# Kernel optimization log

Measured on AMD Instinct MI355X. Metric: run time of the kernel, lower is better.

## Reference

```python
import jax, jax.numpy as jnp
import numpy as np

B, C, H, W = 8, 256, 64, 64
EPS = 1e-5


def _mk_conv_bn(key, oc, ic):
    k = jax.random.split(key, 6)
    return dict(
        w=jax.random.normal(k[0], (oc, ic), jnp.float32) * 0.01,  # trunc-normal approx, stddev 0.01
        b=jnp.zeros((oc,), jnp.float32),
        s=jax.random.uniform(k[1], (oc,), jnp.float32, 0.5, 1.5),   # BN scale
        t=jax.random.normal(k[2], (oc,), jnp.float32) * 0.1,        # BN shift
        m=jax.random.normal(k[3], (oc,), jnp.float32) * 0.1,        # BN running mean
        v=jax.random.uniform(k[4], (oc,), jnp.float32, 0.5, 1.5),   # BN running var
    )


def setup_inputs() -> dict:
    key = jax.random.key(0)
    ks = jax.random.split(key, 6)
    d = {"x": jax.random.normal(ks[0], (B, C, H, W), jnp.float32)}
    for i, (oc, ic) in zip([1, 2, 3, 4], [(C // 8, C), (C // 8, C), (C // 2, C), (C, C // 2)]):
        p = _mk_conv_bn(ks[i], oc, ic)
        for name, val in p.items():
            d[f"{name}{i}"] = val
    d["gamma"] = jnp.asarray(0.5, jnp.float32)
    return d


def _cbn(x, w, b, s, t, m, v, relu=True):
    # conv1x1 + BatchNorm(eval) [+ ReLU]; dropout is identity at inference
    y = jnp.einsum('bchw,oc->bohw', x, w) + b[None, :, None, None]
    scale = (s / jnp.sqrt(v + EPS))[None, :, None, None]
    y = (y - m[None, :, None, None]) * scale + t[None, :, None, None]
    return jax.nn.relu(y) if relu else y


def _maxpool2(x):
    b, c, h, w = x.shape
    return x.reshape(b, c, h // 2, 2, w // 2, 2).max(axis=(3, 5))


def reference(x, w1, b1, s1, t1, m1, v1, w2, b2, s2, t2, m2, v2,
              w3, b3, s3, t3, m3, v3, w4, b4, s4, t4, m4, v4, gamma):
    b, c, h, w = x.shape
    f = _maxpool2(_cbn(x, w1, b1, s1, t1, m1, v1))   # (B, C/8, H/2, W/2)
    g = _cbn(x, w2, b2, s2, t2, m2, v2)              # (B, C/8, H, W)
    hh = _maxpool2(_cbn(x, w3, b3, s3, t3, m3, v3))  # (B, C/2, H/2, W/2)
    hw, hw4 = h * w, (h // 2) * (w // 2)
    f = f.reshape(b, c // 8, hw4).transpose(0, 2, 1)  # (B, HW/4, C/8)
    g = g.reshape(b, c // 8, hw)                      # (B, C/8, HW)
    s = jnp.einsum('bnk,bkm->bnm', f, g)              # (B, HW/4, HW)
    beta = jax.nn.softmax(s, axis=1)                  # softmax over dim=1, as in source
    hh = hh.reshape(b, c // 2, hw4)                   # (B, C/2, HW/4)
    o = jnp.einsum('bcn,bnm->bcm', hh, beta).reshape(b, c // 2, h, w)
    out = _cbn(o, w4, b4, s4, t4, m4, v4, relu=False)
    return gamma * out + x
```

## Files before the change

### kernel.cpp

```cpp
#include <hip/hip_runtime.h>
#include <hip/hip_bf16.h>

#define HW   4096
#define HW4  1024
#define EPS  1e-5f
#define SM_SHIFT 20.0f

typedef __attribute__((ext_vector_type(8)))  short    bf16x8;
typedef __attribute__((ext_vector_type(4)))  float    f32x4;

__device__ __forceinline__ short f2bs(float f) {
    union { float f; unsigned u; } v; v.f = f;
    unsigned r = v.u + 0x7FFFu + ((v.u >> 16) & 1u);
    return (short)(r >> 16);
}
__device__ __forceinline__ int swz64(int r, int c)  { return (r << 6) + ((c ^ (r & 7))  << 3); }
__device__ __forceinline__ int swz128(int r, int c) { return (r << 7) + ((c ^ (r & 15)) << 3); }
__device__ __forceinline__ int p40(int r, int c)    { return r * 40 + c * 8; }

__global__ __launch_bounds__(256) void conv123pool(
    const float* __restrict__ x,
    const float* __restrict__ w1, const float* __restrict__ b1, const float* __restrict__ s1,
    const float* __restrict__ t1, const float* __restrict__ m1, const float* __restrict__ v1,
    const float* __restrict__ w2, const float* __restrict__ b2, const float* __restrict__ s2,
    const float* __restrict__ t2, const float* __restrict__ m2, const float* __restrict__ v2,
    const float* __restrict__ w3, const float* __restrict__ b3, const float* __restrict__ s3,
    const float* __restrict__ t3, const float* __restrict__ m3, const float* __restrict__ v3,
    const float* __restrict__ w4,
    short* __restrict__ w4T,
    short* __restrict__ gbufT, short* __restrict__ fbufT, short* __restrict__ hhbuf)
{
    __shared__ __align__(16) short Wl[96 * 64];
    __shared__ __align__(16) short Xl[128 * 64];
    __shared__ float alB[96], beB[96];

    const int t = threadIdx.x;
    const int lane = t & 63, wv = t >> 6;
    const int quad = lane >> 4, l16 = lane & 15;
    const int ptile = blockIdx.x;
    const int ocg   = blockIdx.y;
    const int bz    = blockIdx.z;
    const int pBase = ptile * 128;
    const int wcol  = (wv & 1) * 32;
    const int woch  = (wv >> 1) * 48;

    if (ocg == 0 && bz == 0) {
        int idx = (ptile * 256 + t) * 4;
        float4 a = *(const float4*)(w4 + idx);
        short4 o;
        o.x = f2bs(a.x); o.y = f2bs(a.y); o.z = f2bs(a.z); o.w = f2bs(a.w);
        *(short4*)&w4T[idx] = o;
    }

    if (t < 96) {
        int j = ocg * 96 + t;
        float pb, ps, ptv, pm, pv;
        if (j < 32)      { pb = b1[j]; ps = s1[j]; ptv = t1[j]; pm = m1[j]; pv = v1[j]; }
        else if (j < 64) { int c = j - 32; pb = b2[c]; ps = s2[c]; ptv = t2[c]; pm = m2[c]; pv = v2[c]; }
        else             { int c = j - 64; pb = b3[c]; ps = s3[c]; ptv = t3[c]; pm = m3[c]; pv = v3[c]; }
        float al = ps * rsqrtf(pv + EPS);
        alB[t] = al; beB[t] = (pb - pm) * al + ptv;
    }

    const f32x4 fzero = {0.f, 0.f, 0.f, 0.f};
    f32x4 acc[3][4];
    #pragma unroll
    for (int i = 0; i < 3; ++i)
        #pragma unroll
        for (int j = 0; j < 4; ++j) acc[i][j] = fzero;

    const int ptOff0 = wcol, ptOff1 = wcol + 16, ptOff2 = wcol + 64, ptOff3 = wcol + 80;
    const int xp  = t & 127, xk8 = t >> 7;
    const float* xBase = x + ((size_t)bz * 256 + xk8 * 32) * HW + pBase + xp;

    float fvA[32], fvB[32];
    #pragma unroll
    for (int i = 0; i < 32; ++i) fvA[i] = xBase[(size_t)i * HW];

#define K1_CHUNK(KC, CUR, NXT)                                                        \
    {                                                                                 \
        _Pragma("unroll")                                                             \
        for (int i = 0; i < 2; ++i) {                                                 \
            int idx = t + i * 256;                                                    \
            if (i == 0 || t < 128) {                                                  \
                int oc = idx >> 2, kb = (idx & 3) * 16;                               \
                int j = ocg * 96 + oc;                                                \
                const float* wp = (j < 32) ? (w1 + j * 256)                           \
                                : (j < 64) ? (w2 + (j - 32) * 256)                    \
                                           : (w3 + (j - 64) * 256);                   \
                wp += (KC) * 64 + kb;                                                 \
                float4 a = *(const float4*)(wp);                                      \
                float4 b = *(const float4*)(wp + 4);                                  \
                float4 c = *(const float4*)(wp + 8);                                  \
                float4 d = *(const float4*)(wp + 12);                                 \
                bf16x8 lo, hi;                                                        \
                lo[0]=f2bs(a.x); lo[1]=f2bs(a.y); lo[2]=f2bs(a.z); lo[3]=f2bs(a.w);   \
                lo[4]=f2bs(b.x); lo[5]=f2bs(b.y); lo[6]=f2bs(b.z); lo[7]=f2bs(b.w);   \
                hi[0]=f2bs(c.x); hi[1]=f2bs(c.y); hi[2]=f2bs(c.z); hi[3]=f2bs(c.w);   \
                hi[4]=f2bs(d.x); hi[5]=f2bs(d.y); hi[6]=f2bs(d.z); hi[7]=f2bs(d.w);   \
                *(bf16x8*)&Wl[swz64(oc, (kb >> 3))]     = lo;                         \
                *(bf16x8*)&Wl[swz64(oc, (kb >> 3) + 1)] = hi;                         \
            }                                                                         \
        }                                                                             \
        if ((KC) < 3) {                                                               \
            const float* xn = xBase + (size_t)(((KC) + 1) * 64) * HW;                 \
            _Pragma("unroll")                                                         \
            for (int i2 = 0; i2 < 32; ++i2) NXT[i2] = xn[(size_t)i2 * HW];            \
        }                                                                             \
        _Pragma("unroll")                                                             \
        for (int c2 = 0; c2 < 4; ++c2) {                                              \
            bf16x8 v;                                                                 \
            _Pragma("unroll")                                                         \
            for (int jj = 0; jj < 8; ++jj) v[jj] = f2bs(CUR[c2 * 8 + jj]);            \
            *(bf16x8*)&Xl[swz64(xp, xk8 * 4 + c2)] = v;                               \
        }                                                                             \
        __syncthreads();                                                              \
        _Pragma("unroll")                                                             \
        for (int kk = 0; kk < 2; ++kk) {                                              \
            bf16x8 bfr[4];                                                            \
            bfr[0] = *(const bf16x8*)&Xl[swz64(ptOff0 + l16, kk * 4 + quad)];         \
            bfr[1] = *(const bf16x8*)&Xl[swz64(ptOff1 + l16, kk * 4 + quad)];         \
            bfr[2] = *(const bf16x8*)&Xl[swz64(ptOff2 + l16, kk * 4 + quad)];         \
            bfr[3] = *(const bf16x8*)&Xl[swz64(ptOff3 + l16, kk * 4 + quad)];         \
            _Pragma("unroll")                                                         \
            for (int tt = 0; tt < 3; ++tt) {                                          \
                bf16x8 afr = *(const bf16x8*)&Wl[swz64(woch + tt*16 + l16, kk*4 + quad)]; \
                _Pragma("unroll")                                                     \
                for (int pt = 0; pt < 4; ++pt)                                        \
                    acc[tt][pt] = __builtin_amdgcn_mfma_f32_16x16x32_bf16(afr, bfr[pt], acc[tt][pt], 0, 0, 0); \
            }                                                                         \
        }                                                                             \
        __syncthreads();                                                              \
    }

    K1_CHUNK(0, fvA, fvB)
    K1_CHUNK(1, fvB, fvA)
    K1_CHUNK(2, fvA, fvB)
    K1_CHUNK(3, fvB, fvA)
#undef K1_CHUNK

    #pragma unroll
    for (int tt = 0; tt < 3; ++tt) {
        #pragma unroll
        for (int r = 0; r < 4; ++r) {
            int ocl = woch + tt * 16 + quad * 4 + r;
            int j = ocg * 96 + ocl;
            float al = alB[ocl], be = beB[ocl];
            float y[4];
            y[0] = fmaxf(acc[tt][0][r] * al + be, 0.f);
            y[1] = fmaxf(acc[tt][1][r] * al + be, 0.f);
            y[2] = fmaxf(acc[tt][2][r] * al + be, 0.f);
            y[3] = fmaxf(acc[tt][3][r] * al + be, 0.f);
            if (j >= 32 && j < 64) {
                size_t mb = (size_t)bz * 4096 + pBase;
                int kk = j - 32;
                gbufT[(mb + ptOff0 + l16) * 32 + kk] = f2bs(y[0]);
                gbufT[(mb + ptOff1 + l16) * 32 + kk] = f2bs(y[1]);
                gbufT[(mb + ptOff2 + l16) * 32 + kk] = f2bs(y[2]);
                gbufT[(mb + ptOff3 + l16) * 32 + kk] = f2bs(y[3]);
            } else {
                #pragma unroll
                for (int c = 0; c < 2; ++c) {
                    float v  = fmaxf(y[c], y[c + 2]);
                    float po = fmaxf(v, __shfl_xor(v, 1));
                    if ((l16 & 1) == 0) {
                        int col = wcol + c * 16 + l16;
                        int n = ptile * 32 + (col >> 1);
                        if (j < 32) fbufT[((size_t)bz * 1024 + n) * 32 + j] = f2bs(po);
                        else        hhbuf[((size_t)bz * 128 + (j - 64)) * HW4 + n] = f2bs(po);
                    }
                }
            }
        }
    }
}

__global__ __launch_bounds__(256, 2) void attn_conv4(
    const short* __restrict__ gbufT,
    const short* __restrict__ fbufT,
    const short* __restrict__ hhbuf,
    const float* __restrict__ x,
    const short* __restrict__ w4T, const float* __restrict__ b4, const float* __restrict__ s4,
    const float* __restrict__ t4, const float* __restrict__ m4, const float* __restrict__ v4,
    const float* __restrict__ gamma, float* __restrict__ out)
{
    __shared__ __align__(16) short smem[24576];
    __shared__ float alB4[256], beB4[256];
    __shared__ float Zl[64];
    short* sT0  = smem;
    short* sT1  = smem + 4096;
    short* hhl0 = smem + 8192;
    short* hhl1 = smem + 16384;
    short* o_l  = smem;
    short* Wl4  = smem + 8192;

    const int t = threadIdx.x;
    const int lane = t & 63, wv = t >> 6;
    const int quad = lane >> 4, l16 = lane & 15;
    const int bz = blockIdx.y;
    const int m0 = blockIdx.x * 64;
    const f32x4 fzero = {0.f, 0.f, 0.f, 0.f};

    {
        float al = s4[t] * rsqrtf(v4[t] + EPS);
        alB4[t] = al; beB4[t] = (b4[t] - m4[t]) * al + t4[t];
    }

    const short* fT = fbufT + (size_t)bz * 1024 * 32;
    const short* hB = hhbuf + (size_t)bz * 128 * HW4;
    const int hrow = t >> 3, hnc = t & 7;

    bf16x8 bg = *(const bf16x8*)&gbufT[((size_t)bz * 4096 + m0 + wv * 16 + l16) * 32 + quad * 8];

    bf16x8 fr[4], hr[4];
    #pragma unroll
    for (int nt = 0; nt < 4; ++nt)
        fr[nt] = *(const bf16x8*)&fT[(nt * 16 + l16) * 32 + quad * 8];
    #pragma unroll
    for (int i = 0; i < 4; ++i)
        hr[i] = *(const bf16x8*)(hB + (size_t)(i * 32 + hrow) * HW4 + hnc * 8);

    float psum = 0.f;
    f32x4 oacc[2][4];
    #pragma unroll
    for (int a = 0; a < 2; ++a)
        #pragma unroll
        for (int b = 0; b < 4; ++b) oacc[a][b] = fzero;

    #pragma unroll 2
    for (int it = 0; it < 16; ++it) {
        const int n0n = ((it + 1) & 15) << 6;
        short* hb = (it & 1) ? hhl1 : hhl0;
        short* sT = (it & 1) ? sT1  : sT0;

        #pragma unroll
        for (int i = 0; i < 4; ++i)
            *(bf16x8*)&hb[swz64(i * 32 + hrow, hnc)] = hr[i];
        #pragma unroll
        for (int i = 0; i < 4; ++i)
            hr[i] = *(const bf16x8*)(hB + (size_t)(i * 32 + hrow) * HW4 + n0n + hnc * 8);

        f32x4 sacc[4];
        #pragma unroll
        for (int nt = 0; nt < 4; ++nt)
            sacc[nt] = __builtin_amdgcn_mfma_f32_16x16x32_bf16(fr[nt], bg, fzero, 0, 0, 0);
        #pragma unroll
        for (int nt = 0; nt < 4; ++nt)
            fr[nt] = *(const bf16x8*)&fT[(n0n + nt * 16 + l16) * 32 + quad * 8];

        #pragma unroll
        for (int nt = 0; nt < 4; ++nt) {
            short4 ev;
            #pragma unroll
            for (int r = 0; r < 4; ++r) {
                float e = __expf(sacc[nt][r] - SM_SHIFT);
                psum += e;
                ((short*)&ev)[r] = f2bs(e);
            }
            *(short4*)&sT[swz64(wv * 16 + l16, nt * 2 + (quad >> 1)) + (quad & 1) * 4] = ev;
        }

        __syncthreads();

        #pragma unroll
        for (int kk = 0; kk < 2; ++kk) {
            bf16x8 ah0 = *(const bf16x8*)&hb[swz64(wv * 32 + l16,      kk * 4 + quad)];
            bf16x8 ah1 = *(const bf16x8*)&hb[swz64(wv * 32 + 16 + l16, kk * 4 + quad)];
            bf16x8 bs[4];
            #pragma unroll
            for (int mt = 0; mt < 4; ++mt)
                bs[mt] = *(const bf16x8*)&sT[swz64(mt * 16 + l16, kk * 4 + quad)];
            #pragma unroll
            for (int mt = 0; mt < 4; ++mt) {
                oacc[0][mt] = __builtin_amdgcn_mfma_f32_16x16x32_bf16(ah0, bs[mt], oacc[0][mt], 0, 0, 0);
                oacc[1][mt] = __builtin_amdgcn_mfma_f32_16x16x32_bf16(ah1, bs[mt], oacc[1][mt], 0, 0, 0);
            }
        }
    }

    psum += __shfl_xor(psum, 16);
    psum += __shfl_xor(psum, 32);
    if (quad == 0) Zl[wv * 16 + l16] = psum;
    __syncthreads();

    #pragma unroll
    for (int mt = 0; mt < 4; ++mt) {
        float iv = 1.0f / Zl[mt * 16 + l16];
        #pragma unroll
        for (int ct2 = 0; ct2 < 2; ++ct2) {
            short4 ov;
            #pragma unroll
            for (int r = 0; r < 4; ++r) ((short*)&ov)[r] = f2bs(oacc[ct2][mt][r] * iv);
            *(short4*)&o_l[swz128(mt * 16 + l16, wv * 4 + ct2 * 2 + (quad >> 1)) + (quad & 1) * 4] = ov;
        }
    }

    f32x4 acc4[4][4];
    #pragma unroll
    for (int i = 0; i < 4; ++i)
        #pragma unroll
        for (int j = 0; j < 4; ++j) acc4[i][j] = fzero;

    const int wrow = t >> 2, wcid = t & 3;
    bf16x8 Wr[4];
    #pragma unroll
    for (int g = 0; g < 4; ++g)
        Wr[g] = *(const bf16x8*)(w4T + (g * 64 + wrow) * 128 + wcid * 8);

    #pragma unroll
    for (int k0i = 0; k0i < 4; ++k0i) {
        const int k0 = k0i * 32;
        __syncthreads();
        #pragma unroll
        for (int g = 0; g < 4; ++g)
            *(bf16x8*)&Wl4[p40(g * 64 + wrow, wcid)] = Wr[g];
        if (k0i < 3) {
            #pragma unroll
            for (int g = 0; g < 4; ++g)
                Wr[g] = *(const bf16x8*)(w4T + (g * 64 + wrow) * 128 + k0 + 32 + wcid * 8);
        }
        __syncthreads();
        bf16x8 bfr[4];
        #pragma unroll
        for (int mt = 0; mt < 4; ++mt)
            bfr[mt] = *(const bf16x8*)&o_l[swz128(mt * 16 + l16, (k0 >> 3) + quad)];
        #pragma unroll
        for (int ot = 0; ot < 4; ++ot) {
            bf16x8 afr = *(const bf16x8*)&Wl4[p40(wv * 64 + ot * 16 + l16, quad)];
            #pragma unroll
            for (int mt = 0; mt < 4; ++mt)
                acc4[ot][mt] = __builtin_amdgcn_mfma_f32_16x16x32_bf16(afr, bfr[mt], acc4[ot][mt], 0, 0, 0);
        }
    }

    float gm = gamma[0];
    #pragma unroll
    for (int ot = 0; ot < 4; ++ot) {
        #pragma unroll
        for (int r = 0; r < 4; ++r) {
            int oc = wv * 64 + ot * 16 + quad * 4 + r;
            float al = alB4[oc], be = beB4[oc];
            #pragma unroll
            for (int mt = 0; mt < 4; ++mt) {
                int p = m0 + mt * 16 + l16;
                float y  = acc4[ot][mt][r] * al + be;
                float xo = x[((size_t)bz * 256 + oc) * HW + p];
                out[((size_t)bz * 256 + oc) * HW + p] = gm * y + xo;
            }
        }
    }
}

extern "C" void kernel_launch(void* const* d_in, const int* in_sizes, int n_in,
                              void* d_out, int out_size, void* d_ws, size_t ws_size,
                              hipStream_t stream)
{
    const float* x  = (const float*)d_in[0];
    const float* w1 = (const float*)d_in[1];
    const float* b1 = (const float*)d_in[2];
    const float* s1 = (const float*)d_in[3];
    const float* t1 = (const float*)d_in[4];
    const float* m1 = (const float*)d_in[5];
    const float* v1 = (const float*)d_in[6];
    const float* w2 = (const float*)d_in[7];
    const float* b2 = (const float*)d_in[8];
    const float* s2 = (const float*)d_in[9];
    const float* t2 = (const float*)d_in[10];
    const float* m2 = (const float*)d_in[11];
    const float* v2 = (const float*)d_in[12];
    const float* w3 = (const float*)d_in[13];
    const float* b3 = (const float*)d_in[14];
    const float* s3 = (const float*)d_in[15];
    const float* t3 = (const float*)d_in[16];
    const float* m3 = (const float*)d_in[17];
    const float* v3 = (const float*)d_in[18];
    const float* w4 = (const float*)d_in[19];
    const float* b4 = (const float*)d_in[20];
    const float* s4 = (const float*)d_in[21];
    const float* t4 = (const float*)d_in[22];
    const float* m4 = (const float*)d_in[23];
    const float* v4 = (const float*)d_in[24];
    const float* gm = (const float*)d_in[25];
    float* out = (float*)d_out;

    short* gbufT = (short*)d_ws;
    short* fbufT = gbufT + (size_t)8 * 4096 * 32;
    short* hhbuf = fbufT + (size_t)8 * 1024 * 32;
    short* w4T   = hhbuf + (size_t)8 * 128 * 1024;

    conv123pool<<<dim3(32, 2, 8), 256, 0, stream>>>(
        x, w1, b1, s1, t1, m1, v1, w2, b2, s2, t2, m2, v2, w3, b3, s3, t3, m3, v3,
        w4, w4T, gbufT, fbufT, hhbuf);
    attn_conv4<<<dim3(64, 8), 256, 0, stream>>>(
        gbufT, fbufT, hhbuf, x, w4T, b4, s4, t4, m4, v4, gm, out);
}
```

Measured before the change: 160.3 us.

## Merge output-channel groups into one 512-thread block to share x tile

The conv123pool kernel previously launched two blocks per pixel tile, one for each 96-channel group, and each loaded the same x tile. Blocks now have 512 threads and cover all 192 output channels, so each x tile is read and converted to bf16 once. The x loads are also reorganized into float2 vector loads. In exchange the grid shrinks to 256 blocks, which lowers parallelism on a large GPU and increases per-block LDS use.

Measured after the change: 158.5 us. No clear change (-1.1%).

```diff
diff --git a/kernel.cpp b/kernel.cpp
--- a/kernel.cpp
+++ b/kernel.cpp
@@ -18,7 +18,7 @@
 __device__ __forceinline__ int swz128(int r, int c) { return (r << 7) + ((c ^ (r & 15)) << 3); }
 __device__ __forceinline__ int p40(int r, int c)    { return r * 40 + c * 8; }
 
-__global__ __launch_bounds__(256) void conv123pool(
+__global__ __launch_bounds__(512) void conv123pool(
     const float* __restrict__ x,
     const float* __restrict__ w1, const float* __restrict__ b1, const float* __restrict__ s1,
     const float* __restrict__ t1, const float* __restrict__ m1, const float* __restrict__ v1,
@@ -30,30 +30,35 @@
     short* __restrict__ w4T,
     short* __restrict__ gbufT, short* __restrict__ fbufT, short* __restrict__ hhbuf)
 {
-    __shared__ __align__(16) short Wl[96 * 64];
+    __shared__ __align__(16) short Wl[192 * 64];
     __shared__ __align__(16) short Xl[128 * 64];
-    __shared__ float alB[96], beB[96];
+    __shared__ float alB[192], beB[192];
 
     const int t = threadIdx.x;
     const int lane = t & 63, wv = t >> 6;
     const int quad = lane >> 4, l16 = lane & 15;
     const int ptile = blockIdx.x;
-    const int ocg   = blockIdx.y;
-    const int bz    = blockIdx.z;
+    const int bz    = blockIdx.y;
     const int pBase = ptile * 128;
     const int wcol  = (wv & 1) * 32;
     const int woch  = (wv >> 1) * 48;
 
-    if (ocg == 0 && bz == 0) {
-        int idx = (ptile * 256 + t) * 4;
-        float4 a = *(const float4*)(w4 + idx);
-        short4 o;
-        o.x = f2bs(a.x); o.y = f2bs(a.y); o.z = f2bs(a.z); o.w = f2bs(a.w);
-        *(short4*)&w4T[idx] = o;
-    }
-
-    if (t < 96) {
-        int j = ocg * 96 + t;
+    const int xp2 = (t & 63) * 2, xkg = t >> 6;
+    const float* xBase = x + ((size_t)bz * 256 + xkg * 8) * HW + pBase + xp2;
+
+    float2 fvA[8], fvB[8];
+    #pragma unroll
+    for (int j = 0; j < 8; ++j) fvA[j] = *(const float2*)(xBase + (size_t)j * HW);
+
+    if (bz == 0) {
+        int idx = (ptile * 512 + t) * 2;
+        float2 a = *(const float2*)(w4 + idx);
+        short2 o; o.x = f2bs(a.x); o.y = f2bs(a.y);
+        *(short2*)&w4T[idx] = o;
+    }
+
+    if (t < 192) {
+        int j = t;
         float pb, ps, ptv, pm, pv;
         if (j < 32)      { pb = b1[j]; ps = s1[j]; ptv = t1[j]; pm = m1[j]; pv = v1[j]; }
         else if (j < 64) { int c = j - 32; pb = b2[c]; ps = s2[c]; ptv = t2[c]; pm = m2[c]; pv = v2[c]; }
@@ -70,24 +75,17 @@
         for (int j = 0; j < 4; ++j) acc[i][j] = fzero;
 
     const int ptOff0 = wcol, ptOff1 = wcol + 16, ptOff2 = wcol + 64, ptOff3 = wcol + 80;
-    const int xp  = t & 127, xk8 = t >> 7;
-    const float* xBase = x + ((size_t)bz * 256 + xk8 * 32) * HW + pBase + xp;
-
-    float fvA[32], fvB[32];
-    #pragma unroll
-    for (int i = 0; i < 32; ++i) fvA[i] = xBase[(size_t)i * HW];
 
 #define K1_CHUNK(KC, CUR, NXT)                                                        \
     {                                                                                 \
         _Pragma("unroll")                                                             \
         for (int i = 0; i < 2; ++i) {                                                 \
-            int idx = t + i * 256;                                                    \
-            if (i == 0 || t < 128) {                                                  \
+            int idx = t + i * 512;                                                    \
+            if (i == 0 || t < 256) {                                                  \
                 int oc = idx >> 2, kb = (idx & 3) * 16;                               \
-                int j = ocg * 96 + oc;                                                \
-                const float* wp = (j < 32) ? (w1 + j * 256)                           \
-                                : (j < 64) ? (w2 + (j - 32) * 256)                    \
-                                           : (w3 + (j - 64) * 256);                   \
+                const float* wp = (oc < 32) ? (w1 + oc * 256)                         \
+                                : (oc < 64) ? (w2 + (oc - 32) * 256)                  \
+                                            : (w3 + (oc - 64) * 256);                 \
                 wp += (KC) * 64 + kb;                                                 \
                 float4 a = *(const float4*)(wp);                                      \
                 float4 b = *(const float4*)(wp + 4);                                  \
@@ -105,14 +103,14 @@
         if ((KC) < 3) {                                                               \
             const float* xn = xBase + (size_t)(((KC) + 1) * 64) * HW;                 \
             _Pragma("unroll")                                                         \
-            for (int i2 = 0; i2 < 32; ++i2) NXT[i2] = xn[(size_t)i2 * HW];            \
+            for (int j2 = 0; j2 < 8; ++j2) NXT[j2] = *(const float2*)(xn + (size_t)j2 * HW); \
         }                                                                             \
-        _Pragma("unroll")                                                             \
-        for (int c2 = 0; c2 < 4; ++c2) {                                              \
-            bf16x8 v;                                                                 \
+        {                                                                             \
+            bf16x8 va, vb;                                                            \
             _Pragma("unroll")                                                         \
-            for (int jj = 0; jj < 8; ++jj) v[jj] = f2bs(CUR[c2 * 8 + jj]);            \
-            *(bf16x8*)&Xl[swz64(xp, xk8 * 4 + c2)] = v;                               \
+            for (int j2 = 0; j2 < 8; ++j2) { va[j2] = f2bs(CUR[j2].x); vb[j2] = f2bs(CUR[j2].y); } \
+            *(bf16x8*)&Xl[swz64(xp2,     xkg)] = va;                                  \
+            *(bf16x8*)&Xl[swz64(xp2 + 1, xkg)] = vb;                                  \
         }                                                                             \
         __syncthreads();                                                              \
         _Pragma("unroll")                                                             \
@@ -143,9 +141,8 @@
     for (int tt = 0; tt < 3; ++tt) {
         #pragma unroll
         for (int r = 0; r < 4; ++r) {
-            int ocl = woch + tt * 16 + quad * 4 + r;
-            int j = ocg * 96 + ocl;
-            float al = alB[ocl], be = beB[ocl];
+            int j = woch + tt * 16 + quad * 4 + r;
+            float al = alB[j], be = beB[j];
             float y[4];
             y[0] = fmaxf(acc[tt][0][r] * al + be, 0.f);
             y[1] = fmaxf(acc[tt][1][r] * al + be, 0.f);
@@ -388,7 +385,7 @@
     short* hhbuf = fbufT + (size_t)8 * 1024 * 32;
     short* w4T   = hhbuf + (size_t)8 * 128 * 1024;
 
-    conv123pool<<<dim3(32, 2, 8), 256, 0, stream>>>(
+    conv123pool<<<dim3(32, 8), 512, 0, stream>>>(
         x, w1, b1, s1, t1, m1, v1, w2, b2, s2, t2, m2, v2, w3, b3, s3, t3, m3, v3,
         w4, w4T, gbufT, fbufT, hhbuf);
     attn_conv4<<<dim3(64, 8), 256, 0, stream>>>(
```
